# Optimization experiments

Measured on AMD Instinct MI355X. Metric: run time of the kernel, lower is better.

## Reference

```python
import jax, jax.numpy as jnp
import numpy as np

E, T, IN, OUT, GS = 8, 2048, 2048, 2048, 64


def setup_inputs() -> dict:
    key = jax.random.key(0)
    k1, k2, k3, k4, k5 = jax.random.split(key, 5)
    x = jax.random.normal(k1, (T, IN), dtype=jnp.float32)
    # int4 codes in [0,16): stored unpacked as int32 for the reference
    qweight = jax.random.randint(k2, (E, IN, OUT), 0, 16, dtype=jnp.int32)
    G = IN // GS  # quant groups along the reduction dim
    scales = jax.random.uniform(k3, (E, G, OUT), jnp.float32, minval=0.005, maxval=0.02)
    zeros = jax.random.normal(k4, (E, G, OUT), jnp.float32) * 0.01
    scales_and_zeros = jnp.stack([scales, zeros], axis=-1)  # [E, G, OUT, 2]
    # tokens sorted by expert: per-expert counts are diffs of sorted cut points, sum == T
    cuts = jnp.sort(jax.random.randint(k5, (E - 1,), 0, T + 1, dtype=jnp.int32))
    bounds = jnp.concatenate([jnp.zeros((1,), jnp.int32), cuts, jnp.full((1,), T, jnp.int32)])
    tokens_per_expert = jnp.diff(bounds).astype(jnp.int32)  # [E]
    return {
        "x": x,
        "qweight": qweight,
        "scales_and_zeros": scales_and_zeros,
        "tokens_per_expert": tokens_per_expert,
        "group_size": GS,
    }


def reference(x, qweight, scales_and_zeros, tokens_per_expert, group_size):
    """Grouped (per-expert) int4 dequant + GEMM over an expert-sorted token matrix.

    Math of aten._weight_int4pack_mm per expert e over each quant group g:
        W_e[k, n] = (q_e[k, n] - 8) * scale_e[g, n] + zero_e[g, n],  g = k // group_size
        out[rows_e] = x[rows_e] @ W_e
    where rows_e is the contiguous slice given by cumsum(tokens_per_expert).
    """
    n_exp, in_f, out_f = qweight.shape
    n_tok = x.shape[0]
    G = in_f // group_size

    # dequantize all expert weights: [E, IN, OUT]
    q = qweight.reshape(n_exp, G, group_size, out_f).astype(x.dtype)
    scales = scales_and_zeros[..., 0][:, :, None, :]  # [E, G, 1, OUT]
    zeros = scales_and_zeros[..., 1][:, :, None, :]   # [E, G, 1, OUT]
    W = ((q - 8.0) * scales + zeros).reshape(n_exp, in_f, out_f)

    # expert id per token from the cumsum boundaries (tokens are expert-sorted)
    cum = jnp.cumsum(tokens_per_expert)                                # [E]
    eid = jnp.searchsorted(cum, jnp.arange(n_tok), side="right")       # [T]
    onehot = (eid[:, None] == jnp.arange(n_exp)[None, :]).astype(x.dtype)  # [T, E]

    # dispatch -> per-expert GEMM -> combine (jit-safe grouped GEMM)
    xe = jnp.einsum("te,ti->eti", onehot, x)       # [E, T, IN]
    ye = jnp.einsum("eti,eio->eto", xe, W)         # [E, T, OUT]
    out = jnp.einsum("te,eto->to", onehot, ye)     # [T, OUT]
    return out
```

## Files before the change

kernel.cpp:

```cpp
#include <hip/hip_runtime.h>
#include <hip/hip_bf16.h>

constexpr int NE  = 8;
constexpr int T   = 2048;
constexpr int IN  = 2048;
constexpr int OUT = 2048;
constexpr int GS  = 64;
constexpr int G   = IN / GS;

constexpr int BM = 128;
constexpr int BN = 64;
constexpr int BK = 64;
constexpr int KSPLIT = 2;
constexpr int KCH = IN / KSPLIT;
constexpr int LDB = BK + 8;

using short8  = __attribute__((ext_vector_type(8))) short;
using floatx4 = __attribute__((ext_vector_type(4))) float;

__global__ __launch_bounds__(256)
void cvt_x_bf16(const float* __restrict__ x, __hip_bfloat16* __restrict__ xb) {
    const int i = (blockIdx.x * 256 + threadIdx.x) * 4;
    const float4 v = *(const float4*)(x + i);
    union { unsigned long long u; __hip_bfloat162 h2[2]; } p;
    p.h2[0] = __float22bfloat162_rn(float2{v.x, v.y});
    p.h2[1] = __float22bfloat162_rn(float2{v.z, v.w});
    *(unsigned long long*)(xb + i) = p.u;
}

__global__ __launch_bounds__(256, 4)
void hqq_grouped_gemm(const __hip_bfloat16* __restrict__ xb,
                      const int*   __restrict__ qw,
                      const float* __restrict__ snz,
                      const int*   __restrict__ tpe,
                      float* __restrict__ out) {
    const int tid = threadIdx.x;
    const int e   = blockIdx.z >> 1;
    const int kh  = blockIdx.z & 1;
    const int tm  = blockIdx.y;
    const int n0  = blockIdx.x * BN;

    int b0 = 0;
    for (int i = 0; i < NE; ++i) {
        int c = tpe[i];
        if (i < e) b0 += c;
    }
    const int b1 = b0 + tpe[e];
    const int row0 = b0 + tm * BM;
    if (row0 >= b1) return;

    __shared__ __hip_bfloat16 Bs[BN][LDB];

    floatx4 acc[2][4];
#pragma unroll
    for (int i = 0; i < 2; ++i)
#pragma unroll
        for (int j = 0; j < 4; ++j)
            acc[i][j] = (floatx4){0.f, 0.f, 0.f, 0.f};

    const int bn_ = tid & 63;
    const int bk0 = (tid >> 6) * 8;

    const int lane = tid & 63;
    const int wid  = tid >> 6;
    const int wm = wid * 32;
    const int lm = lane & 15;
    const int lk = (lane >> 4) * 8;

    const int*    qbase  = qw + (size_t)e * IN * OUT + n0 + bn_;
    const float2* szbase = (const float2*)snz + (size_t)e * G * OUT + n0 + bn_;

    const int kbeg  = kh * KCH;
    const int ntile = KCH / BK;

    int    qv[16];
    float2 szv;

    auto issue = [&](int k0) {
        szv = szbase[(size_t)(k0 >> 6) * OUT];
#pragma unroll
        for (int p = 0; p < 2; ++p) {
            const int* qp = qbase + (size_t)(k0 + bk0 + p * 32) * OUT;
#pragma unroll
            for (int j = 0; j < 8; ++j)
                qv[p * 8 + j] = qp[(size_t)j * OUT];
        }
    };

    issue(kbeg);

    for (int t = 0; t < ntile; ++t) {
        const int k0 = kbeg + t * BK;

        const float s = szv.x;
        const float c = szv.y - 8.0f * s;
#pragma unroll
        for (int p = 0; p < 2; ++p) {
            union { short8 v; __hip_bfloat162 h2[4]; } pb;
#pragma unroll
            for (int j = 0; j < 4; ++j) {
                const float f0 = (float)qv[p * 8 + 2 * j]     * s + c;
                const float f1 = (float)qv[p * 8 + 2 * j + 1] * s + c;
                pb.h2[j] = __float22bfloat162_rn(float2{f0, f1});
            }
            *(short8*)&Bs[bn_][bk0 + p * 32] = pb.v;
        }

        __syncthreads();

        const int kn = (t + 1 < ntile) ? k0 + BK : k0;
        issue(kn);

#pragma unroll
        for (int ks = 0; ks < BK; ks += 32) {
            short8 af[2], bfr[4];
#pragma unroll
            for (int i = 0; i < 2; ++i) {
                const int row = row0 + wm + i * 16 + lm;
                const int rr  = row < b1 ? row : (b1 - 1);
                af[i] = *(const short8*)(xb + (size_t)rr * IN + k0 + ks + lk);
            }
#pragma unroll
            for (int j = 0; j < 4; ++j)
                bfr[j] = *(const short8*)&Bs[j * 16 + lm][ks + lk];
#pragma unroll
            for (int i = 0; i < 2; ++i)
#pragma unroll
                for (int j = 0; j < 4; ++j)
                    acc[i][j] = __builtin_amdgcn_mfma_f32_16x16x32_bf16(
                        af[i], bfr[j], acc[i][j], 0, 0, 0);
        }

        __syncthreads();
    }

    const int lq = (lane >> 4) * 4;
#pragma unroll
    for (int i = 0; i < 2; ++i) {
#pragma unroll
        for (int r = 0; r < 4; ++r) {
            const int row = row0 + wm + i * 16 + lq + r;
            if (row < b1) {
                float* op = out + (size_t)row * OUT + n0 + lm;
#pragma unroll
                for (int j = 0; j < 4; ++j)
                    atomicAdd(op + j * 16, acc[i][j][r]);
            }
        }
    }
}

extern "C" void kernel_launch(void* const* d_in, const int* in_sizes, int n_in,
                              void* d_out, int out_size, void* d_ws, size_t ws_size,
                              hipStream_t stream) {
    const float* x   = (const float*)d_in[0];
    const int*   qw  = (const int*)d_in[1];
    const float* snz = (const float*)d_in[2];
    const int*   tpe = (const int*)d_in[3];
    float* out = (float*)d_out;
    __hip_bfloat16* xb = (__hip_bfloat16*)d_ws;

    hipMemsetAsync(out, 0, (size_t)out_size * sizeof(float), stream);

    cvt_x_bf16<<<(T * IN) / (256 * 4), 256, 0, stream>>>(x, xb);

    dim3 grid(OUT / BN, T / BM, NE * KSPLIT);
    hqq_grouped_gemm<<<grid, 256, 0, stream>>>(xb, qw, snz, tpe, out);
}
```

Baseline: 268.0 us.

## Dequantize a 512-deep weight slab once per block and loop over all expert rows

Each block now owns one expert, one 64-column strip and a 512-wide K chunk. It dequantizes that whole weight slab into shared memory once, then its four waves sweep every 32-row tile of the expert's tokens against it. Before, each 128-row tile block reloaded and re-dequantized the int4 weights, which re-read the dominant weight traffic once per row tile. The cost is a 64x520 bf16 shared buffer that lowers occupancy, work serialized inside blocks with uneven per-expert token counts, and a 4-way K split that doubles the atomic adds to the output.

```diff
diff --git a/kernel.cpp b/kernel.cpp
--- a/kernel.cpp
+++ b/kernel.cpp
@@ -8,12 +8,10 @@
 constexpr int GS  = 64;
 constexpr int G   = IN / GS;
 
-constexpr int BM = 128;
 constexpr int BN = 64;
-constexpr int BK = 64;
-constexpr int KSPLIT = 2;
-constexpr int KCH = IN / KSPLIT;
-constexpr int LDB = BK + 8;
+constexpr int KC = 512;
+constexpr int KSPLIT = IN / KC;
+constexpr int LDB = KC + 8;
 
 using short8  = __attribute__((ext_vector_type(8))) short;
 using floatx4 = __attribute__((ext_vector_type(4))) float;
@@ -28,16 +26,15 @@
     *(unsigned long long*)(xb + i) = p.u;
 }
 
-__global__ __launch_bounds__(256, 4)
+__global__ __launch_bounds__(256, 2)
 void hqq_grouped_gemm(const __hip_bfloat16* __restrict__ xb,
                       const int*   __restrict__ qw,
                       const float* __restrict__ snz,
                       const int*   __restrict__ tpe,
                       float* __restrict__ out) {
     const int tid = threadIdx.x;
-    const int e   = blockIdx.z >> 1;
-    const int kh  = blockIdx.z & 1;
-    const int tm  = blockIdx.y;
+    const int e   = blockIdx.z;
+    const int kc  = blockIdx.y * KC;
     const int n0  = blockIdx.x * BN;
 
     int b0 = 0;
@@ -46,80 +43,70 @@
         if (i < e) b0 += c;
     }
     const int b1 = b0 + tpe[e];
-    const int row0 = b0 + tm * BM;
-    if (row0 >= b1) return;
+    const int nrows = b1 - b0;
+    if (nrows <= 0) return;
 
     __shared__ __hip_bfloat16 Bs[BN][LDB];
 
-    floatx4 acc[2][4];
+    const int bn_ = tid & 63;
+    const int ko  = (tid >> 6) * 8;
+    const int*    qcol  = qw + (size_t)e * IN * OUT + (size_t)kc * OUT + n0 + bn_;
+    const float2* szcol = (const float2*)snz + (size_t)e * G * OUT + n0 + bn_;
+
+#pragma unroll 4
+    for (int i = 0; i < 16; ++i) {
+        const int kb = ko + 32 * i;
+        const int g  = (kc + kb) >> 6;
+        const float2 sz = szcol[(size_t)g * OUT];
+        const float s = sz.x;
+        const float c = sz.y - 8.0f * s;
+        const int* qp = qcol + (size_t)kb * OUT;
+        int q[8];
 #pragma unroll
-    for (int i = 0; i < 2; ++i)
+        for (int j = 0; j < 8; ++j)
+            q[j] = qp[(size_t)j * OUT];
+        union { short8 v; __hip_bfloat162 h2[4]; } pb;
 #pragma unroll
-        for (int j = 0; j < 4; ++j)
-            acc[i][j] = (floatx4){0.f, 0.f, 0.f, 0.f};
+        for (int j = 0; j < 4; ++j) {
+            const float f0 = (float)q[2 * j]     * s + c;
+            const float f1 = (float)q[2 * j + 1] * s + c;
+            pb.h2[j] = __float22bfloat162_rn(float2{f0, f1});
+        }
+        *(short8*)&Bs[bn_][kb] = pb.v;
+    }
 
-    const int bn_ = tid & 63;
-    const int bk0 = (tid >> 6) * 8;
+    __syncthreads();
 
     const int lane = tid & 63;
     const int wid  = tid >> 6;
-    const int wm = wid * 32;
     const int lm = lane & 15;
     const int lk = (lane >> 4) * 8;
+    const int lq = (lane >> 4) * 4;
 
-    const int*    qbase  = qw + (size_t)e * IN * OUT + n0 + bn_;
-    const float2* szbase = (const float2*)snz + (size_t)e * G * OUT + n0 + bn_;
+    for (int mt = wid; mt * 32 < nrows; mt += 4) {
+        const int r0 = b0 + mt * 32;
 
-    const int kbeg  = kh * KCH;
-    const int ntile = KCH / BK;
-
-    int    qv[16];
-    float2 szv;
-
-    auto issue = [&](int k0) {
-        szv = szbase[(size_t)(k0 >> 6) * OUT];
+        const __hip_bfloat16* abase[2];
 #pragma unroll
-        for (int p = 0; p < 2; ++p) {
-            const int* qp = qbase + (size_t)(k0 + bk0 + p * 32) * OUT;
-#pragma unroll
-            for (int j = 0; j < 8; ++j)
-                qv[p * 8 + j] = qp[(size_t)j * OUT];
-        }
-    };
-
-    issue(kbeg);
-
-    for (int t = 0; t < ntile; ++t) {
-        const int k0 = kbeg + t * BK;
-
-        const float s = szv.x;
-        const float c = szv.y - 8.0f * s;
-#pragma unroll
-        for (int p = 0; p < 2; ++p) {
-            union { short8 v; __hip_bfloat162 h2[4]; } pb;
-#pragma unroll
-            for (int j = 0; j < 4; ++j) {
-                const float f0 = (float)qv[p * 8 + 2 * j]     * s + c;
-                const float f1 = (float)qv[p * 8 + 2 * j + 1] * s + c;
-                pb.h2[j] = __float22bfloat162_rn(float2{f0, f1});
-            }
-            *(short8*)&Bs[bn_][bk0 + p * 32] = pb.v;
+        for (int i = 0; i < 2; ++i) {
+            const int row = r0 + i * 16 + lm;
+            const int rr  = row < b1 ? row : (b1 - 1);
+            abase[i] = xb + (size_t)rr * IN + kc + lk;
         }
 
-        __syncthreads();
+        floatx4 acc[2][4];
+#pragma unroll
+        for (int i = 0; i < 2; ++i)
+#pragma unroll
+            for (int j = 0; j < 4; ++j)
+                acc[i][j] = (floatx4){0.f, 0.f, 0.f, 0.f};
 
-        const int kn = (t + 1 < ntile) ? k0 + BK : k0;
-        issue(kn);
-
-#pragma unroll
-        for (int ks = 0; ks < BK; ks += 32) {
+#pragma unroll 4
+        for (int ks = 0; ks < KC; ks += 32) {
             short8 af[2], bfr[4];
 #pragma unroll
-            for (int i = 0; i < 2; ++i) {
-                const int row = row0 + wm + i * 16 + lm;
-                const int rr  = row < b1 ? row : (b1 - 1);
-                af[i] = *(const short8*)(xb + (size_t)rr * IN + k0 + ks + lk);
-            }
+            for (int i = 0; i < 2; ++i)
+                af[i] = *(const short8*)(abase[i] + ks);
 #pragma unroll
             for (int j = 0; j < 4; ++j)
                 bfr[j] = *(const short8*)&Bs[j * 16 + lm][ks + lk];
@@ -131,20 +118,17 @@
                         af[i], bfr[j], acc[i][j], 0, 0, 0);
         }
 
-        __syncthreads();
-    }
-
-    const int lq = (lane >> 4) * 4;
 #pragma unroll
-    for (int i = 0; i < 2; ++i) {
+        for (int i = 0; i < 2; ++i) {
 #pragma unroll
-        for (int r = 0; r < 4; ++r) {
-            const int row = row0 + wm + i * 16 + lq + r;
-            if (row < b1) {
-                float* op = out + (size_t)row * OUT + n0 + lm;
+            for (int r = 0; r < 4; ++r) {
+                const int row = r0 + i * 16 + lq + r;
+                if (row < b1) {
+                    float* op = out + (size_t)row * OUT + n0 + lm;
 #pragma unroll
-                for (int j = 0; j < 4; ++j)
-                    atomicAdd(op + j * 16, acc[i][j][r]);
+                    for (int j = 0; j < 4; ++j)
+                        atomicAdd(op + j * 16, acc[i][j][r]);
+                }
             }
         }
     }
@@ -164,6 +148,6 @@
 
     cvt_x_bf16<<<(T * IN) / (256 * 4), 256, 0, stream>>>(x, xb);
 
-    dim3 grid(OUT / BN, T / BM, NE * KSPLIT);
+    dim3 grid(OUT / BN, KSPLIT, NE);
     hqq_grouped_gemm<<<grid, 256, 0, stream>>>(xb, qw, snz, tpe, out);
 }
```

Result: no change. 271.6 us (+1.3%).

## Split dequant into separate pass and stage A/B via global_load_lds

Applied to the files above, without the earlier changes.

Moves int4 dequantization out of the GEMM into a standalone kernel that writes transposed bf16 weights to workspace. The GEMM then stages both the activation and weight tiles into LDS using direct global-to-LDS loads. It drops the K-split, which removes the output memset and replaces the atomics with plain stores. The cost is an extra full pass that reads every expert's int32 weights and writes 8x2048x2048 bf16 to workspace, plus a GEMM grid with half as many blocks.

```diff
diff --git a/kernel.cpp b/kernel.cpp
--- a/kernel.cpp
+++ b/kernel.cpp
@@ -11,12 +11,15 @@
 constexpr int BM = 128;
 constexpr int BN = 64;
 constexpr int BK = 64;
-constexpr int KSPLIT = 2;
-constexpr int KCH = IN / KSPLIT;
-constexpr int LDB = BK + 8;
 
 using short8  = __attribute__((ext_vector_type(8))) short;
 using floatx4 = __attribute__((ext_vector_type(4))) float;
+
+__device__ __forceinline__ void gld_lds16(const void* g, void* l) {
+    __builtin_amdgcn_global_load_lds(
+        (const __attribute__((address_space(1))) unsigned int*)g,
+        (__attribute__((address_space(3))) unsigned int*)l, 16, 0, 0);
+}
 
 __global__ __launch_bounds__(256)
 void cvt_x_bf16(const float* __restrict__ x, __hip_bfloat16* __restrict__ xb) {
@@ -28,15 +31,45 @@
     *(unsigned long long*)(xb + i) = p.u;
 }
 
+__global__ __launch_bounds__(256)
+void dequant_wt(const int* __restrict__ qw, const float* __restrict__ snz,
+                __hip_bfloat16* __restrict__ wt) {
+    const int e  = blockIdx.z;
+    const int k0 = blockIdx.y * 64;
+    const int n  = blockIdx.x * 256 + threadIdx.x;
+    const int g  = k0 >> 6;
+
+    const float2 sz = ((const float2*)snz)[(size_t)e * G * OUT + (size_t)g * OUT + n];
+    const float s = sz.x;
+    const float c = sz.y - 8.0f * s;
+
+    const int* qp = qw + (size_t)e * IN * OUT + (size_t)k0 * OUT + n;
+    __hip_bfloat16* wp = wt + (size_t)e * OUT * IN + (size_t)n * IN + k0;
+
+#pragma unroll
+    for (int kk = 0; kk < 64; kk += 8) {
+        int q[8];
+#pragma unroll
+        for (int j = 0; j < 8; ++j)
+            q[j] = qp[(size_t)(kk + j) * OUT];
+        union { short8 v; __hip_bfloat162 h2[4]; } pb;
+#pragma unroll
+        for (int j = 0; j < 4; ++j) {
+            const float f0 = (float)q[2 * j]     * s + c;
+            const float f1 = (float)q[2 * j + 1] * s + c;
+            pb.h2[j] = __float22bfloat162_rn(float2{f0, f1});
+        }
+        *(short8*)(wp + kk) = pb.v;
+    }
+}
+
 __global__ __launch_bounds__(256, 4)
-void hqq_grouped_gemm(const __hip_bfloat16* __restrict__ xb,
-                      const int*   __restrict__ qw,
-                      const float* __restrict__ snz,
-                      const int*   __restrict__ tpe,
-                      float* __restrict__ out) {
+void hqq_gemm(const __hip_bfloat16* __restrict__ xb,
+              const __hip_bfloat16* __restrict__ wt,
+              const int* __restrict__ tpe,
+              float* __restrict__ out) {
     const int tid = threadIdx.x;
-    const int e   = blockIdx.z >> 1;
-    const int kh  = blockIdx.z & 1;
+    const int e   = blockIdx.z;
     const int tm  = blockIdx.y;
     const int n0  = blockIdx.x * BN;
 
@@ -49,7 +82,18 @@
     const int row0 = b0 + tm * BM;
     if (row0 >= b1) return;
 
-    __shared__ __hip_bfloat16 Bs[BN][LDB];
+    __shared__ __hip_bfloat16 As[BM * BK];
+    __shared__ __hip_bfloat16 Bs[BN * BK];
+
+    const int sm = tid >> 3;
+    const int sk = (tid & 7) * 8;
+
+    const int lane = tid & 63;
+    const int wid  = tid >> 6;
+    const int wm = wid * 32;
+    const int lm = lane & 15;
+    const int lk = (lane >> 4) * 8;
+    const int lq = (lane >> 4) * 4;
 
     floatx4 acc[2][4];
 #pragma unroll
@@ -58,71 +102,35 @@
         for (int j = 0; j < 4; ++j)
             acc[i][j] = (floatx4){0.f, 0.f, 0.f, 0.f};
 
-    const int bn_ = tid & 63;
-    const int bk0 = (tid >> 6) * 8;
+    int arow[4];
+#pragma unroll
+    for (int I = 0; I < 4; ++I) {
+        int r = row0 + sm + 32 * I;
+        arow[I] = r < T ? r : (T - 1);
+    }
+    const __hip_bfloat16* wbase = wt + (size_t)e * OUT * IN + (size_t)(n0 + sm) * IN;
 
-    const int lane = tid & 63;
-    const int wid  = tid >> 6;
-    const int wm = wid * 32;
-    const int lm = lane & 15;
-    const int lk = (lane >> 4) * 8;
-
-    const int*    qbase  = qw + (size_t)e * IN * OUT + n0 + bn_;
-    const float2* szbase = (const float2*)snz + (size_t)e * G * OUT + n0 + bn_;
-
-    const int kbeg  = kh * KCH;
-    const int ntile = KCH / BK;
-
-    int    qv[16];
-    float2 szv;
-
-    auto issue = [&](int k0) {
-        szv = szbase[(size_t)(k0 >> 6) * OUT];
+    for (int k0 = 0; k0 < IN; k0 += BK) {
 #pragma unroll
-        for (int p = 0; p < 2; ++p) {
-            const int* qp = qbase + (size_t)(k0 + bk0 + p * 32) * OUT;
+        for (int I = 0; I < 4; ++I)
+            gld_lds16(xb + (size_t)arow[I] * IN + k0 + sk,
+                      &As[(sm + 32 * I) * BK + sk]);
 #pragma unroll
-            for (int j = 0; j < 8; ++j)
-                qv[p * 8 + j] = qp[(size_t)j * OUT];
-        }
-    };
-
-    issue(kbeg);
-
-    for (int t = 0; t < ntile; ++t) {
-        const int k0 = kbeg + t * BK;
-
-        const float s = szv.x;
-        const float c = szv.y - 8.0f * s;
-#pragma unroll
-        for (int p = 0; p < 2; ++p) {
-            union { short8 v; __hip_bfloat162 h2[4]; } pb;
-#pragma unroll
-            for (int j = 0; j < 4; ++j) {
-                const float f0 = (float)qv[p * 8 + 2 * j]     * s + c;
-                const float f1 = (float)qv[p * 8 + 2 * j + 1] * s + c;
-                pb.h2[j] = __float22bfloat162_rn(float2{f0, f1});
-            }
-            *(short8*)&Bs[bn_][bk0 + p * 32] = pb.v;
-        }
+        for (int I = 0; I < 2; ++I)
+            gld_lds16(wbase + (size_t)(32 * I) * IN + k0 + sk,
+                      &Bs[(sm + 32 * I) * BK + sk]);
 
         __syncthreads();
-
-        const int kn = (t + 1 < ntile) ? k0 + BK : k0;
-        issue(kn);
 
 #pragma unroll
         for (int ks = 0; ks < BK; ks += 32) {
             short8 af[2], bfr[4];
 #pragma unroll
-            for (int i = 0; i < 2; ++i) {
-                const int row = row0 + wm + i * 16 + lm;
-                const int rr  = row < b1 ? row : (b1 - 1);
-                af[i] = *(const short8*)(xb + (size_t)rr * IN + k0 + ks + lk);
-            }
+            for (int i = 0; i < 2; ++i)
+                af[i] = *(const short8*)&As[(wm + i * 16 + lm) * BK + ks + lk];
 #pragma unroll
             for (int j = 0; j < 4; ++j)
-                bfr[j] = *(const short8*)&Bs[j * 16 + lm][ks + lk];
+                bfr[j] = *(const short8*)&Bs[(j * 16 + lm) * BK + ks + lk];
 #pragma unroll
             for (int i = 0; i < 2; ++i)
 #pragma unroll
@@ -134,7 +142,6 @@
         __syncthreads();
     }
 
-    const int lq = (lane >> 4) * 4;
 #pragma unroll
     for (int i = 0; i < 2; ++i) {
 #pragma unroll
@@ -144,7 +151,7 @@
                 float* op = out + (size_t)row * OUT + n0 + lm;
 #pragma unroll
                 for (int j = 0; j < 4; ++j)
-                    atomicAdd(op + j * 16, acc[i][j][r]);
+                    op[j * 16] = acc[i][j][r];
             }
         }
     }
@@ -158,12 +165,14 @@
     const float* snz = (const float*)d_in[2];
     const int*   tpe = (const int*)d_in[3];
     float* out = (float*)d_out;
+
+    const size_t xb_bytes = (size_t)T * IN * sizeof(__hip_bfloat16);
     __hip_bfloat16* xb = (__hip_bfloat16*)d_ws;
-
-    hipMemsetAsync(out, 0, (size_t)out_size * sizeof(float), stream);
+    __hip_bfloat16* wt = (__hip_bfloat16*)((char*)d_ws + xb_bytes);
 
     cvt_x_bf16<<<(T * IN) / (256 * 4), 256, 0, stream>>>(x, xb);
 
-    dim3 grid(OUT / BN, T / BM, NE * KSPLIT);
-    hqq_grouped_gemm<<<grid, 256, 0, stream>>>(xb, qw, snz, tpe, out);
+    dequant_wt<<<dim3(OUT / 256, IN / 64, NE), 256, 0, stream>>>(qw, snz, wt);
+
+    hqq_gemm<<<dim3(OUT / BN, T / BM, NE), 256, 0, stream>>>(xb, wt, tpe, out);
 }
```

New measurement: 322.7 us. 1.2x slower.
